# Performance work log

Hardware: AMD Instinct MI355X
Metric: run time of the kernel (lower is better)

The kernel has to match this reference:

```python
import jax, jax.numpy as jnp
import numpy as np

SIZE = 640
FPN_STRIDES = (8, 16, 32, 64, 128)
REG_MAX = 16
NUM_CLASSES = 80
TOPK = 45


def _build_anchors():
    pts, boxes, strides = [], [], []
    for s in FPN_STRIDES:
        h, w = SIZE // s, SIZE // s
        y, x = np.meshgrid(np.arange(h), np.arange(w), indexing='ij')
        yf = y.ravel().astype(np.float32)
        xf = x.ravel().astype(np.float32)
        pts.append(np.stack([(yf + 0.5) * s, (xf + 0.5) * s], -1))
        boxes.append(np.stack([yf * s, xf * s, (yf + 1) * s, (xf + 1) * s], -1))
        strides.append(np.full(h * w, s, np.float32))
    return (jnp.asarray(np.concatenate(pts), jnp.float32),
            jnp.asarray(np.concatenate(boxes), jnp.float32),
            jnp.asarray(np.concatenate(strides), jnp.float32))


ANCHOR_PTS, ANCHOR_BOXES, STRIDES = _build_anchors()
NUM_ANCHORS = ANCHOR_PTS.shape[0]  # 8525


def _iou(b1, b2):
    # elementwise IoU over trailing dim 4 in (y1, x1, y2, x2); axes are symmetric
    ty = jnp.maximum(b1[..., 0], b2[..., 0])
    tx = jnp.maximum(b1[..., 1], b2[..., 1])
    by = jnp.minimum(b1[..., 2], b2[..., 2])
    bx = jnp.minimum(b1[..., 3], b2[..., 3])
    inter = jnp.clip(by - ty, 0.0) * jnp.clip(bx - tx, 0.0)
    a1 = (b1[..., 2] - b1[..., 0]) * (b1[..., 3] - b1[..., 1])
    a2 = (b2[..., 2] - b2[..., 0]) * (b2[..., 3] - b2[..., 1])
    return inter / (a1 + a2 - inter)


def _assign_single(gt_cls, gt_bbox, pred_d):
    # gt_cls: (N,), gt_bbox: (N,4), pred_d: (4,A)
    A, N, C = NUM_ANCHORS, gt_bbox.shape[0], NUM_CLASSES
    pts, boxes, strides = ANCHOR_PTS, ANCHOR_BOXES, STRIDES
    centers = (gt_bbox[:, :2] + gt_bbox[:, 2:]) / 2
    dist = jnp.linalg.norm(centers[:, None, :] - pts[None, :, :], axis=-1)  # (N,A)
    _, k_ind = jax.lax.top_k(-dist, TOPK)  # (N,K) nearest anchors
    kb = boxes[k_ind]  # (N,K,4)
    Dg = _iou(gt_bbox[:, None, :], kb)  # (N,K)
    tg = Dg.mean(1) + Dg.std(1, ddof=1)  # torch .std() is unbiased
    ap = pts[k_ind]  # (N,K,2)
    inside = ((gt_bbox[:, None, 0] <= ap[..., 0]) & (ap[..., 0] <= gt_bbox[:, None, 2]) &
              (gt_bbox[:, None, 1] <= ap[..., 1]) & (ap[..., 1] <= gt_bbox[:, None, 3]))
    valid = (Dg >= tg[:, None]) & inside  # (N,K)
    n_idx = jnp.broadcast_to(jnp.arange(N, dtype=jnp.int32)[:, None], (N, TOPK))
    pri = jnp.where(valid, n_idx, -1).ravel()
    a_flat = k_ind.ravel()
    win_d = jnp.full((A,), -1, jnp.int32).at[a_flat].max(pri)
    wb = gt_bbox[jnp.clip(win_d, 0)]  # (A,4)
    gt_d = jnp.stack([(pts[:, 0] - wb[:, 0]) / strides,
                      (pts[:, 1] - wb[:, 1]) / strides,
                      (wb[:, 2] - pts[:, 0]) / strides,
                      (wb[:, 3] - pts[:, 1]) / strides], 0)  # (4,A) = [dtop,dleft,dbottom,dright]
    gt_dfl = jnp.where(win_d[None, :] >= 0, gt_d, jnp.inf)
    cls_pair = gt_cls.astype(jnp.int32)[n_idx]  # (N,K)
    ca = (cls_pair * A + k_ind).ravel()
    win_q = jnp.full((C * A,), -1, jnp.int32).at[ca].max(pri).reshape(C, A)
    gbq = gt_bbox[jnp.clip(win_q, 0)]  # (C,A,4)
    # _overlap_tlbr: decode(gt_d)*stride around anchor point, clamped -> clipped gt box
    box1 = jnp.clip(gbq, 0.0, float(SIZE))  # (C,A,4)
    rd = pred_d * strides[None, :]  # (4,A) raw offsets
    box2 = jnp.stack([jnp.clip(pts[:, 0] - rd[0], 0.0, float(SIZE)),
                      jnp.clip(pts[:, 1] - rd[1], 0.0, float(SIZE)),
                      jnp.clip(pts[:, 0] + rd[2], 0.0, float(SIZE)),
                      jnp.clip(pts[:, 1] + rd[3], 0.0, float(SIZE))], -1)  # (A,4)
    q = _iou(box1, box2[None, :, :])  # (C,A)
    gt_qfl = jnp.where(win_q >= 0, q, 0.0)
    return gt_qfl, gt_dfl


def setup_inputs() -> dict:
    key = jax.random.key(0)
    k1, k2, k3, k4 = jax.random.split(key, 4)
    B, N = 16, 64
    tl = jax.random.uniform(k1, (B, N, 2), jnp.float32, 0.0, SIZE - 64.0)
    wh = jax.random.uniform(k2, (B, N, 2), jnp.float32, 16.0, 256.0)
    br = jnp.minimum(tl + wh, float(SIZE))
    gt_bboxes = jnp.concatenate([tl, br], -1)  # (y1,x1,y2,x2)
    gt_clses = jax.random.randint(k3, (B, N), 0, NUM_CLASSES)
    pred_reg = jax.random.normal(k4, (B, 4, REG_MAX + 1, NUM_ANCHORS), jnp.float32)
    return {"gt_clses_batch": gt_clses, "gt_bboxes_batch": gt_bboxes,
            "pred_reg_batch": pred_reg}


def reference(gt_clses_batch, gt_bboxes_batch, pred_reg_batch):
    p = jax.nn.softmax(pred_reg_batch, axis=2)
    rng = jnp.arange(REG_MAX + 1, dtype=p.dtype).reshape(1, 1, -1, 1)
    pred_d = (p * rng).sum(2)  # (B,4,A) integral distribution -> expected offsets
    qfl, dfl = jax.vmap(_assign_single)(gt_clses_batch, gt_bboxes_batch, pred_d)
    return qfl, dfl, ANCHOR_PTS, STRIDES
```

## Files before the change

kernel.cpp:

```cpp
#include <hip/hip_runtime.h>
#include <math.h>
#include <float.h>

#define A_TOTAL 8525
#define NUM_B   16
#define NUM_N   64
#define NUM_C   80
#define K_TOP   45
#define SIZE_F  640.0f

#define UNASSIGNED_SENTINEL 1.0e30f

#define CUTOFF_KEY 0x43000000u
#define NBINS_PAD  2304
#define CAND_MAX   768

#define QFL_FLOATS  ((size_t)NUM_B * NUM_C * A_TOTAL)
#define DFL_FLOATS  ((size_t)NUM_B * 4 * A_TOTAL)
#define MASK_WORDS  (NUM_B * A_TOTAL)
#define MASK_VEC4   ((MASK_WORDS * 2) / 4)
#define QFL_VEC4    (QFL_FLOATS / 4)
#define DFL_VEC4    (DFL_FLOATS / 4)

__device__ __forceinline__ void anchor_decode(int a, float& py, float& px, float& s,
                                              float& qy0, float& qx0, float& qy1, float& qx1) {
    int rel, w; float sf;
    if (a < 6400)      { rel = a;        w = 80; sf = 8.f;   }
    else if (a < 8000) { rel = a - 6400; w = 40; sf = 16.f;  }
    else if (a < 8400) { rel = a - 8000; w = 20; sf = 32.f;  }
    else if (a < 8500) { rel = a - 8400; w = 10; sf = 64.f;  }
    else               { rel = a - 8500; w = 5;  sf = 128.f; }
    int y = rel / w, x = rel - y * w;
    float yf = (float)y, xf = (float)x;
    py  = (yf + 0.5f) * sf;  px  = (xf + 0.5f) * sf;
    qy0 = yf * sf;           qx0 = xf * sf;
    qy1 = (yf + 1.f) * sf;   qx1 = (xf + 1.f) * sf;
    s = sf;
}

__device__ __forceinline__ unsigned int dist_key_yx(int yy, int xx, float s,
                                                    float cy, float cx) {
    float py = __fmul_rn(__fadd_rn((float)yy, 0.5f), s);
    float px = __fmul_rn(__fadd_rn((float)xx, 0.5f), s);
    float dy = __fadd_rn(cy, -py);
    float dx = __fadd_rn(cx, -px);
    float v = sqrtf(__fadd_rn(__fmul_rn(dy, dy), __fmul_rn(dx, dx)));
    return __float_as_uint(v);
}

__device__ __forceinline__ float iou_box(float ay0, float ax0, float ay1, float ax1,
                                         float by0, float bx0, float by1, float bx1) {
    float ty = fmaxf(ay0, by0), tx = fmaxf(ax0, bx0);
    float by = fminf(ay1, by1), bx = fminf(ax1, bx1);
    float ih = fmaxf(__fadd_rn(by, -ty), 0.f);
    float iw = fmaxf(__fadd_rn(bx, -tx), 0.f);
    float inter = __fmul_rn(ih, iw);
    float a1 = __fmul_rn(__fadd_rn(ay1, -ay0), __fadd_rn(ax1, -ax0));
    float a2 = __fmul_rn(__fadd_rn(by1, -by0), __fadd_rn(bx1, -bx0));
    return inter / __fadd_rn(__fadd_rn(a1, a2), -inter);
}

__global__ __launch_bounds__(256) void prep_kernel(unsigned long long* __restrict__ mask,
                                                   float* __restrict__ qfl,
                                                   float* __restrict__ dfl,
                                                   float* __restrict__ opts,
                                                   float* __restrict__ ostr) {
    size_t gid = (size_t)blockIdx.x * 256 + threadIdx.x;
    size_t nthreads = (size_t)gridDim.x * 256;

    const uint4 z4 = make_uint4(0u, 0u, 0u, 0u);
    uint4* q4 = (uint4*)qfl;
    for (size_t i = gid; i < QFL_VEC4; i += nthreads)
        q4[i] = z4;

    const unsigned int su = __float_as_uint(UNASSIGNED_SENTINEL);
    const uint4 s4 = make_uint4(su, su, su, su);
    uint4* d4 = (uint4*)dfl;
    for (size_t i = gid; i < DFL_VEC4; i += nthreads)
        d4[i] = s4;

    uint4* m4 = (uint4*)mask;
    for (size_t i = gid; i < MASK_VEC4; i += nthreads)
        m4[i] = z4;

    for (size_t a = gid; a < A_TOTAL; a += nthreads) {
        float py, px, s, q0, q1, q2, q3;
        anchor_decode((int)a, py, px, s, q0, q1, q2, q3);
        opts[2 * a]     = py;
        opts[2 * a + 1] = px;
        ostr[a]         = s;
    }
}

__global__ __launch_bounds__(256) void assign_kernel(const float* __restrict__ gt_bbox,
                                                     unsigned long long* __restrict__ mask) {
    __shared__ unsigned int hist[NBINS_PAD];
    __shared__ unsigned int wtot[4];
    __shared__ unsigned int cand_key[CAND_MAX];
    __shared__ int          cand_idx[CAND_MAX];
    __shared__ int          s_candn;
    __shared__ int          s_B;
    __shared__ int          sel[K_TOP];
    __shared__ float        dg[K_TOP];
    __shared__ float        s_tg;

    const int   LH[5] = {80, 40, 20, 10, 5};
    const int   LB[5] = {0, 6400, 8000, 8400, 8500};
    const float LS[5] = {8.f, 16.f, 32.f, 64.f, 128.f};

    int tid = threadIdx.x;
    int lane = tid & 63, wid = tid >> 6;
    int b = blockIdx.x >> 6;
    int n = blockIdx.x & 63;
    const float* gb = gt_bbox + (size_t)(b * NUM_N + n) * 4;
    float g0 = gb[0], g1 = gb[1], g2 = gb[2], g3 = gb[3];
    float cy = __fmul_rn(__fadd_rn(g0, g2), 0.5f);
    float cx = __fmul_rn(__fadd_rn(g1, g3), 0.5f);

    int wy0[5], wx0[5], wnc[5], wcl[5];
#pragma unroll
    for (int l = 0; l < 5; ++l) {
        float s = LS[l]; int H = LH[l];
        int y0 = (int)((cy - 68.f) / s) - 1; if (y0 < 0) y0 = 0;
        int y1 = (int)((cy + 68.f) / s) + 1; if (y1 > H - 1) y1 = H - 1;
        int x0 = (int)((cx - 68.f) / s) - 1; if (x0 < 0) x0 = 0;
        int x1 = (int)((cx + 68.f) / s) + 1; if (x1 > H - 1) x1 = H - 1;
        wy0[l] = y0; wx0[l] = x0;
        wnc[l] = x1 - x0 + 1;
        wcl[l] = (y1 - y0 + 1) * wnc[l];
    }

    for (int i = tid; i < NBINS_PAD; i += 256) hist[i] = 0u;
    if (tid == 0) s_candn = 0;
    __syncthreads();

#pragma unroll
    for (int l = 0; l < 5; ++l) {
        int nc = wnc[l], cells = wcl[l];
        for (int t = tid; t < cells; t += 256) {
            int r = t / nc, c = t - r * nc;
            unsigned int key = dist_key_yx(wy0[l] + r, wx0[l] + c, LS[l], cy, cx);
            if (key < CUTOFF_KEY) atomicAdd(&hist[key >> 19], 1u);
        }
    }
    __syncthreads();

    unsigned int psum = 0;
    int base = tid * 9;
#pragma unroll
    for (int k = 0; k < 9; ++k) psum += hist[base + k];
    unsigned int x = psum;
    for (int off = 1; off < 64; off <<= 1) {
        unsigned int y = __shfl_up(x, off, 64);
        if (lane >= off) x += y;
    }
    if (lane == 63) wtot[wid] = x;
    __syncthreads();
    unsigned int wbase = 0;
    for (int w = 0; w < 4; ++w) wbase += (w < wid) ? wtot[w] : 0u;
    unsigned int inc = wbase + x;
    unsigned int exc = inc - psum;
    if (exc < (unsigned)K_TOP && inc >= (unsigned)K_TOP) {
        unsigned int cum = exc;
        int bbin = base;
        while (cum + hist[bbin] < (unsigned)K_TOP) { cum += hist[bbin]; ++bbin; }
        s_B = bbin;
    }
    __syncthreads();

    int B = s_B;
#pragma unroll
    for (int l = 0; l < 5; ++l) {
        int nc = wnc[l], cells = wcl[l];
        for (int t = tid; t < cells; t += 256) {
            int r = t / nc, c = t - r * nc;
            int yy = wy0[l] + r, xx = wx0[l] + c;
            unsigned int key = dist_key_yx(yy, xx, LS[l], cy, cx);
            if (key < CUTOFF_KEY && (int)(key >> 19) <= B) {
                int pos = atomicAdd(&s_candn, 1);
                if (pos < CAND_MAX) {
                    cand_key[pos] = key;
                    cand_idx[pos] = LB[l] + yy * LH[l] + xx;
                }
            }
        }
    }
    __syncthreads();

    int M = s_candn < CAND_MAX ? s_candn : CAND_MAX;
    for (int i = tid; i < M; i += 256) {
        unsigned int ki = cand_key[i]; int ii = cand_idx[i];
        int rank = 0;
        for (int j = 0; j < M; ++j) {
            unsigned int kj = cand_key[j]; int ij = cand_idx[j];
            rank += (kj < ki || (kj == ki && ij < ii)) ? 1 : 0;
        }
        if (rank < K_TOP) sel[rank] = ii;
    }
    __syncthreads();

    if (tid < K_TOP) {
        int a = sel[tid];
        float py, px, s, q0, q1, q2, q3;
        anchor_decode(a, py, px, s, q0, q1, q2, q3);
        dg[tid] = iou_box(g0, g1, g2, g3, q0, q1, q2, q3);
    }
    __syncthreads();
    if (tid == 0) {
        float sum = 0.f;
        for (int k = 0; k < K_TOP; ++k) sum = __fadd_rn(sum, dg[k]);
        float mean = sum / (float)K_TOP;
        float ss = 0.f;
        for (int k = 0; k < K_TOP; ++k) {
            float d = __fadd_rn(dg[k], -mean);
            ss = __fadd_rn(ss, __fmul_rn(d, d));
        }
        s_tg = __fadd_rn(mean, sqrtf(ss / (float)(K_TOP - 1)));
    }
    __syncthreads();
    if (tid < K_TOP) {
        int a = sel[tid];
        float py, px, s, q0, q1, q2, q3;
        anchor_decode(a, py, px, s, q0, q1, q2, q3);
        bool inside = (g0 <= py) && (py <= g2) && (g1 <= px) && (px <= g3);
        if (inside && dg[tid] >= s_tg) {
            atomicOr(&mask[(size_t)b * A_TOTAL + a], 1ull << n);
        }
    }
}

__global__ __launch_bounds__(256) void output_kernel(const int* __restrict__ gt_cls,
                                                     const float* __restrict__ gt_bbox,
                                                     const float* __restrict__ pred_reg,
                                                     const unsigned long long* __restrict__ mask,
                                                     float* __restrict__ qfl,
                                                     float* __restrict__ dfl) {
    __shared__ float s_gb[NUM_N * 4];
    __shared__ float s_gc[NUM_N * 4];
    __shared__ int   s_cls[NUM_N];

    int tid = threadIdx.x;
    int b = blockIdx.y;
    if (tid < NUM_N * 4) {
        float v = gt_bbox[(size_t)b * NUM_N * 4 + tid];
        s_gb[tid] = v;
        s_gc[tid] = fminf(fmaxf(v, 0.f), SIZE_F);
    }
    if (tid < NUM_N) s_cls[tid] = gt_cls[b * NUM_N + tid];
    __syncthreads();

    int a = blockIdx.x * 256 + tid;
    if (a >= A_TOTAL) return;

    unsigned long long m64 = mask[(size_t)b * A_TOTAL + a];
    if (m64 == 0ull) return;

    float* dflp = dfl + (size_t)b * 4 * A_TOTAL + a;
    float* qflp = qfl + (size_t)b * NUM_C * A_TOTAL + a;

    float py, px, s, q0, q1, q2, q3;
    anchor_decode(a, py, px, s, q0, q1, q2, q3);

    float rd[4];
    const float* pr = pred_reg + (size_t)b * 4 * 17 * A_TOTAL + a;
#pragma unroll
    for (int d = 0; d < 4; ++d) {
        float xv[17];
#pragma unroll
        for (int j = 0; j < 17; ++j) xv[j] = pr[(size_t)(d * 17 + j) * A_TOTAL];
        float m = xv[0];
#pragma unroll
        for (int j = 1; j < 17; ++j) m = fmaxf(m, xv[j]);
        float S = 0.f, dot = 0.f;
#pragma unroll
        for (int j = 0; j < 17; ++j) {
            float t = __expf(xv[j] - m);
            S += t;
            dot += t * (float)j;
        }
        rd[d] = (dot / S) * s;
    }
    float b2y0 = fminf(fmaxf(py - rd[0], 0.f), SIZE_F);
    float b2x0 = fminf(fmaxf(px - rd[1], 0.f), SIZE_F);
    float b2y1 = fminf(fmaxf(py + rd[2], 0.f), SIZE_F);
    float b2x1 = fminf(fmaxf(px + rd[3], 0.f), SIZE_F);

    {
        int n = 63 - __clzll(m64);
        dflp[0]            = (py - s_gb[n * 4 + 0]) / s;
        dflp[A_TOTAL]      = (px - s_gb[n * 4 + 1]) / s;
        dflp[2 * A_TOTAL]  = (s_gb[n * 4 + 2] - py) / s;
        dflp[3 * A_TOTAL]  = (s_gb[n * 4 + 3] - px) / s;
    }

    unsigned long long seen0 = 0ull, seen1 = 0ull;
    unsigned long long mm = m64;
    while (mm) {
        int n = 63 - __clzll(mm);
        mm &= ~(1ull << n);
        int c = s_cls[n];
        bool done;
        if (c < 64) {
            unsigned long long bit = 1ull << c;
            done = (seen0 & bit) != 0ull; seen0 |= bit;
        } else {
            unsigned long long bit = 1ull << (c - 64);
            done = (seen1 & bit) != 0ull; seen1 |= bit;
        }
        if (!done) {
            qflp[(size_t)c * A_TOTAL] = iou_box(s_gc[n * 4 + 0], s_gc[n * 4 + 1],
                                                s_gc[n * 4 + 2], s_gc[n * 4 + 3],
                                                b2y0, b2x0, b2y1, b2x1);
        }
    }
}

extern "C" void kernel_launch(void* const* d_in, const int* in_sizes, int n_in,
                              void* d_out, int out_size, void* d_ws, size_t ws_size,
                              hipStream_t stream) {
    const int*   gt_cls   = (const int*)d_in[0];
    const float* gt_bbox  = (const float*)d_in[1];
    const float* pred_reg = (const float*)d_in[2];

    float* qfl  = (float*)d_out;
    float* dfl  = qfl + QFL_FLOATS;
    float* opts = dfl + DFL_FLOATS;
    float* ostr = opts + (size_t)A_TOTAL * 2;

    unsigned long long* mask = (unsigned long long*)d_ws;

    hipLaunchKernelGGL(prep_kernel, dim3(2048), dim3(256), 0, stream,
                       mask, qfl, dfl, opts, ostr);
    hipLaunchKernelGGL(assign_kernel, dim3(NUM_B * NUM_N), dim3(256), 0, stream, gt_bbox, mask);
    hipLaunchKernelGGL(output_kernel, dim3((A_TOTAL + 255) / 256, NUM_B), dim3(256), 0, stream,
                       gt_cls, gt_bbox, pred_reg, mask, qfl, dfl);
}
```

Baseline: 112.0 us.

## Fold output zero-fill into assign kernel and compact assigned anchors into worklist

The large qfl/dfl initialization and anchor-point writes move from the prep kernel into the assign kernel. There they overlap with the per-GT top-k selection instead of running as a separate bandwidth-bound pass, and prep now only clears the mask. The assign kernel also appends each newly assigned (batch, anchor) pair to a global worklist via atomicAdd, so the output kernel walks only assigned anchors with a grid-stride loop instead of scanning all of them. This adds an atomic counter and makes the output kernel stage all batches' GT data into shared memory per block.

```diff
diff --git a/kernel.cpp b/kernel.cpp
--- a/kernel.cpp
+++ b/kernel.cpp
@@ -18,9 +18,13 @@
 #define QFL_FLOATS  ((size_t)NUM_B * NUM_C * A_TOTAL)
 #define DFL_FLOATS  ((size_t)NUM_B * 4 * A_TOTAL)
 #define MASK_WORDS  (NUM_B * A_TOTAL)
+#define MASK_BYTES  ((size_t)MASK_WORDS * 8)
 #define MASK_VEC4   ((MASK_WORDS * 2) / 4)
 #define QFL_VEC4    (QFL_FLOATS / 4)
 #define DFL_VEC4    (DFL_FLOATS / 4)
+#define WL_CAP      (NUM_B * NUM_N * K_TOP)
+
+#define ASSIGN_BLOCKS (NUM_B * NUM_N)
 
 __device__ __forceinline__ void anchor_decode(int a, float& py, float& px, float& s,
                                               float& qy0, float& qx0, float& qy1, float& qx1) {
@@ -61,39 +65,24 @@
 }
 
 __global__ __launch_bounds__(256) void prep_kernel(unsigned long long* __restrict__ mask,
-                                                   float* __restrict__ qfl,
-                                                   float* __restrict__ dfl,
-                                                   float* __restrict__ opts,
-                                                   float* __restrict__ ostr) {
+                                                   int* __restrict__ wcount) {
     size_t gid = (size_t)blockIdx.x * 256 + threadIdx.x;
     size_t nthreads = (size_t)gridDim.x * 256;
-
+    if (gid == 0) *wcount = 0;
+    uint4* m4 = (uint4*)mask;
     const uint4 z4 = make_uint4(0u, 0u, 0u, 0u);
-    uint4* q4 = (uint4*)qfl;
-    for (size_t i = gid; i < QFL_VEC4; i += nthreads)
-        q4[i] = z4;
-
-    const unsigned int su = __float_as_uint(UNASSIGNED_SENTINEL);
-    const uint4 s4 = make_uint4(su, su, su, su);
-    uint4* d4 = (uint4*)dfl;
-    for (size_t i = gid; i < DFL_VEC4; i += nthreads)
-        d4[i] = s4;
-
-    uint4* m4 = (uint4*)mask;
     for (size_t i = gid; i < MASK_VEC4; i += nthreads)
         m4[i] = z4;
-
-    for (size_t a = gid; a < A_TOTAL; a += nthreads) {
-        float py, px, s, q0, q1, q2, q3;
-        anchor_decode((int)a, py, px, s, q0, q1, q2, q3);
-        opts[2 * a]     = py;
-        opts[2 * a + 1] = px;
-        ostr[a]         = s;
-    }
 }
 
 __global__ __launch_bounds__(256) void assign_kernel(const float* __restrict__ gt_bbox,
-                                                     unsigned long long* __restrict__ mask) {
+                                                     unsigned long long* __restrict__ mask,
+                                                     int* __restrict__ wcount,
+                                                     int* __restrict__ wlist,
+                                                     float* __restrict__ qfl,
+                                                     float* __restrict__ dfl,
+                                                     float* __restrict__ opts,
+                                                     float* __restrict__ ostr) {
     __shared__ unsigned int hist[NBINS_PAD];
     __shared__ unsigned int wtot[4];
     __shared__ unsigned int cand_key[CAND_MAX];
@@ -109,6 +98,31 @@
     const float LS[5] = {8.f, 16.f, 32.f, 64.f, 128.f};
 
     int tid = threadIdx.x;
+
+    {
+        size_t gid = (size_t)blockIdx.x * 256 + tid;
+        const size_t nthreads = (size_t)ASSIGN_BLOCKS * 256;
+
+        const uint4 z4 = make_uint4(0u, 0u, 0u, 0u);
+        uint4* q4 = (uint4*)qfl;
+        for (size_t i = gid; i < QFL_VEC4; i += nthreads)
+            q4[i] = z4;
+
+        const unsigned int su = __float_as_uint(UNASSIGNED_SENTINEL);
+        const uint4 s4 = make_uint4(su, su, su, su);
+        uint4* d4 = (uint4*)dfl;
+        for (size_t i = gid; i < DFL_VEC4; i += nthreads)
+            d4[i] = s4;
+
+        for (size_t a = gid; a < A_TOTAL; a += nthreads) {
+            float py, px, s, q0, q1, q2, q3;
+            anchor_decode((int)a, py, px, s, q0, q1, q2, q3);
+            opts[2 * a]     = py;
+            opts[2 * a + 1] = px;
+            ostr[a]         = s;
+        }
+    }
+
     int lane = tid & 63, wid = tid >> 6;
     int b = blockIdx.x >> 6;
     int n = blockIdx.x & 63;
@@ -224,7 +238,12 @@
         anchor_decode(a, py, px, s, q0, q1, q2, q3);
         bool inside = (g0 <= py) && (py <= g2) && (g1 <= px) && (px <= g3);
         if (inside && dg[tid] >= s_tg) {
-            atomicOr(&mask[(size_t)b * A_TOTAL + a], 1ull << n);
+            unsigned long long old =
+                atomicOr(&mask[(size_t)b * A_TOTAL + a], 1ull << n);
+            if (old == 0ull) {
+                int p = atomicAdd(wcount, 1);
+                wlist[p] = b * A_TOTAL + a;
+            }
         }
     }
 }
@@ -233,84 +252,88 @@
                                                      const float* __restrict__ gt_bbox,
                                                      const float* __restrict__ pred_reg,
                                                      const unsigned long long* __restrict__ mask,
+                                                     const int* __restrict__ wcount,
+                                                     const int* __restrict__ wlist,
                                                      float* __restrict__ qfl,
                                                      float* __restrict__ dfl) {
-    __shared__ float s_gb[NUM_N * 4];
-    __shared__ float s_gc[NUM_N * 4];
-    __shared__ int   s_cls[NUM_N];
+    __shared__ float s_gb[NUM_B * NUM_N * 4];
+    __shared__ float s_gc[NUM_B * NUM_N * 4];
+    __shared__ int   s_cls[NUM_B * NUM_N];
 
     int tid = threadIdx.x;
-    int b = blockIdx.y;
-    if (tid < NUM_N * 4) {
-        float v = gt_bbox[(size_t)b * NUM_N * 4 + tid];
-        s_gb[tid] = v;
-        s_gc[tid] = fminf(fmaxf(v, 0.f), SIZE_F);
-    }
-    if (tid < NUM_N) s_cls[tid] = gt_cls[b * NUM_N + tid];
-    __syncthreads();
-
-    int a = blockIdx.x * 256 + tid;
-    if (a >= A_TOTAL) return;
-
-    unsigned long long m64 = mask[(size_t)b * A_TOTAL + a];
-    if (m64 == 0ull) return;
-
-    float* dflp = dfl + (size_t)b * 4 * A_TOTAL + a;
-    float* qflp = qfl + (size_t)b * NUM_C * A_TOTAL + a;
-
-    float py, px, s, q0, q1, q2, q3;
-    anchor_decode(a, py, px, s, q0, q1, q2, q3);
-
-    float rd[4];
-    const float* pr = pred_reg + (size_t)b * 4 * 17 * A_TOTAL + a;
-#pragma unroll
-    for (int d = 0; d < 4; ++d) {
-        float xv[17];
-#pragma unroll
-        for (int j = 0; j < 17; ++j) xv[j] = pr[(size_t)(d * 17 + j) * A_TOTAL];
-        float m = xv[0];
-#pragma unroll
-        for (int j = 1; j < 17; ++j) m = fmaxf(m, xv[j]);
-        float S = 0.f, dot = 0.f;
-#pragma unroll
-        for (int j = 0; j < 17; ++j) {
-            float t = __expf(xv[j] - m);
-            S += t;
-            dot += t * (float)j;
-        }
-        rd[d] = (dot / S) * s;
-    }
-    float b2y0 = fminf(fmaxf(py - rd[0], 0.f), SIZE_F);
-    float b2x0 = fminf(fmaxf(px - rd[1], 0.f), SIZE_F);
-    float b2y1 = fminf(fmaxf(py + rd[2], 0.f), SIZE_F);
-    float b2x1 = fminf(fmaxf(px + rd[3], 0.f), SIZE_F);
-
-    {
-        int n = 63 - __clzll(m64);
-        dflp[0]            = (py - s_gb[n * 4 + 0]) / s;
-        dflp[A_TOTAL]      = (px - s_gb[n * 4 + 1]) / s;
-        dflp[2 * A_TOTAL]  = (s_gb[n * 4 + 2] - py) / s;
-        dflp[3 * A_TOTAL]  = (s_gb[n * 4 + 3] - px) / s;
-    }
-
-    unsigned long long seen0 = 0ull, seen1 = 0ull;
-    unsigned long long mm = m64;
-    while (mm) {
-        int n = 63 - __clzll(mm);
-        mm &= ~(1ull << n);
-        int c = s_cls[n];
-        bool done;
-        if (c < 64) {
-            unsigned long long bit = 1ull << c;
-            done = (seen0 & bit) != 0ull; seen0 |= bit;
-        } else {
-            unsigned long long bit = 1ull << (c - 64);
-            done = (seen1 & bit) != 0ull; seen1 |= bit;
-        }
-        if (!done) {
-            qflp[(size_t)c * A_TOTAL] = iou_box(s_gc[n * 4 + 0], s_gc[n * 4 + 1],
-                                                s_gc[n * 4 + 2], s_gc[n * 4 + 3],
-                                                b2y0, b2x0, b2y1, b2x1);
+    for (int i = tid; i < NUM_B * NUM_N * 4; i += 256) {
+        float v = gt_bbox[i];
+        s_gb[i] = v;
+        s_gc[i] = fminf(fmaxf(v, 0.f), SIZE_F);
+    }
+    for (int i = tid; i < NUM_B * NUM_N; i += 256) s_cls[i] = gt_cls[i];
+    __syncthreads();
+
+    int total = *wcount;
+    for (int i = blockIdx.x * 256 + tid; i < total; i += gridDim.x * 256) {
+        int e = wlist[i];
+        int b = e / A_TOTAL;
+        int a = e - b * A_TOTAL;
+        unsigned long long m64 = mask[e];
+
+        float py, px, s, q0, q1, q2, q3;
+        anchor_decode(a, py, px, s, q0, q1, q2, q3);
+
+        float* dflp = dfl + (size_t)b * 4 * A_TOTAL + a;
+        float* qflp = qfl + (size_t)b * NUM_C * A_TOTAL + a;
+
+        float rd[4];
+        const float* pr = pred_reg + (size_t)b * 4 * 17 * A_TOTAL + a;
+#pragma unroll
+        for (int d = 0; d < 4; ++d) {
+            float xv[17];
+#pragma unroll
+            for (int j = 0; j < 17; ++j) xv[j] = pr[(size_t)(d * 17 + j) * A_TOTAL];
+            float m = xv[0];
+#pragma unroll
+            for (int j = 1; j < 17; ++j) m = fmaxf(m, xv[j]);
+            float S = 0.f, dot = 0.f;
+#pragma unroll
+            for (int j = 0; j < 17; ++j) {
+                float t = __expf(xv[j] - m);
+                S += t;
+                dot += t * (float)j;
+            }
+            rd[d] = (dot / S) * s;
+        }
+        float b2y0 = fminf(fmaxf(py - rd[0], 0.f), SIZE_F);
+        float b2x0 = fminf(fmaxf(px - rd[1], 0.f), SIZE_F);
+        float b2y1 = fminf(fmaxf(py + rd[2], 0.f), SIZE_F);
+        float b2x1 = fminf(fmaxf(px + rd[3], 0.f), SIZE_F);
+
+        {
+            int n = 63 - __clzll(m64);
+            const float* g = s_gb + (size_t)(b * NUM_N + n) * 4;
+            dflp[0]            = (py - g[0]) / s;
+            dflp[A_TOTAL]      = (px - g[1]) / s;
+            dflp[2 * A_TOTAL]  = (g[2] - py) / s;
+            dflp[3 * A_TOTAL]  = (g[3] - px) / s;
+        }
+
+        unsigned long long seen0 = 0ull, seen1 = 0ull;
+        unsigned long long mm = m64;
+        while (mm) {
+            int n = 63 - __clzll(mm);
+            mm &= ~(1ull << n);
+            int c = s_cls[b * NUM_N + n];
+            bool done;
+            if (c < 64) {
+                unsigned long long bit = 1ull << c;
+                done = (seen0 & bit) != 0ull; seen0 |= bit;
+            } else {
+                unsigned long long bit = 1ull << (c - 64);
+                done = (seen1 & bit) != 0ull; seen1 |= bit;
+            }
+            if (!done) {
+                const float* g = s_gc + (size_t)(b * NUM_N + n) * 4;
+                qflp[(size_t)c * A_TOTAL] = iou_box(g[0], g[1], g[2], g[3],
+                                                    b2y0, b2x0, b2y1, b2x1);
+            }
         }
     }
 }
@@ -328,10 +351,12 @@
     float* ostr = opts + (size_t)A_TOTAL * 2;
 
     unsigned long long* mask = (unsigned long long*)d_ws;
-
-    hipLaunchKernelGGL(prep_kernel, dim3(2048), dim3(256), 0, stream,
-                       mask, qfl, dfl, opts, ostr);
-    hipLaunchKernelGGL(assign_kernel, dim3(NUM_B * NUM_N), dim3(256), 0, stream, gt_bbox, mask);
-    hipLaunchKernelGGL(output_kernel, dim3((A_TOTAL + 255) / 256, NUM_B), dim3(256), 0, stream,
-                       gt_cls, gt_bbox, pred_reg, mask, qfl, dfl);
-}
+    int* wcount = (int*)((char*)d_ws + MASK_BYTES);
+    int* wlist  = wcount + 1;
+
+    hipLaunchKernelGGL(prep_kernel, dim3(64), dim3(256), 0, stream, mask, wcount);
+    hipLaunchKernelGGL(assign_kernel, dim3(ASSIGN_BLOCKS), dim3(256), 0, stream,
+                       gt_bbox, mask, wcount, wlist, qfl, dfl, opts, ostr);
+    hipLaunchKernelGGL(output_kernel, dim3(256), dim3(256), 0, stream,
+                       gt_cls, gt_bbox, pred_reg, mask, wcount, wlist, qfl, dfl);
+}
```

Result: slower. 137.4 us (+22.7%).

## Fuse output zero-fill into assign kernel and split softmax per direction

Applied to the files above, without the earlier changes.

Moves the large qfl zeroing, dfl sentinel fill and anchor output writes from the prep kernel into the assign kernel, so this bulk store traffic overlaps with the assign kernel's histogram/top-k work. The prep kernel now only clears the mask. The output kernel is remapped so each of the four wavefronts computes the 17-bin softmax for one regression direction over 64 anchors. Results go through shared memory, and wavefront 0 then writes the IoU scores. This gives four times more threads for the softmax loads, at the cost of an extra barrier and idle wavefronts during the qfl scatter.

```diff
diff --git a/kernel.cpp b/kernel.cpp
--- a/kernel.cpp
+++ b/kernel.cpp
@@ -21,6 +21,8 @@
 #define MASK_VEC4   ((MASK_WORDS * 2) / 4)
 #define QFL_VEC4    (QFL_FLOATS / 4)
 #define DFL_VEC4    (DFL_FLOATS / 4)
+
+#define ASSIGN_BLOCKS (NUM_B * NUM_N)
 
 __device__ __forceinline__ void anchor_decode(int a, float& py, float& px, float& s,
                                               float& qy0, float& qx0, float& qy1, float& qx1) {
@@ -60,40 +62,21 @@
     return inter / __fadd_rn(__fadd_rn(a1, a2), -inter);
 }
 
-__global__ __launch_bounds__(256) void prep_kernel(unsigned long long* __restrict__ mask,
-                                                   float* __restrict__ qfl,
-                                                   float* __restrict__ dfl,
-                                                   float* __restrict__ opts,
-                                                   float* __restrict__ ostr) {
+__global__ __launch_bounds__(256) void prep_kernel(unsigned long long* __restrict__ mask) {
     size_t gid = (size_t)blockIdx.x * 256 + threadIdx.x;
     size_t nthreads = (size_t)gridDim.x * 256;
-
+    uint4* m4 = (uint4*)mask;
     const uint4 z4 = make_uint4(0u, 0u, 0u, 0u);
-    uint4* q4 = (uint4*)qfl;
-    for (size_t i = gid; i < QFL_VEC4; i += nthreads)
-        q4[i] = z4;
-
-    const unsigned int su = __float_as_uint(UNASSIGNED_SENTINEL);
-    const uint4 s4 = make_uint4(su, su, su, su);
-    uint4* d4 = (uint4*)dfl;
-    for (size_t i = gid; i < DFL_VEC4; i += nthreads)
-        d4[i] = s4;
-
-    uint4* m4 = (uint4*)mask;
     for (size_t i = gid; i < MASK_VEC4; i += nthreads)
         m4[i] = z4;
-
-    for (size_t a = gid; a < A_TOTAL; a += nthreads) {
-        float py, px, s, q0, q1, q2, q3;
-        anchor_decode((int)a, py, px, s, q0, q1, q2, q3);
-        opts[2 * a]     = py;
-        opts[2 * a + 1] = px;
-        ostr[a]         = s;
-    }
 }
 
 __global__ __launch_bounds__(256) void assign_kernel(const float* __restrict__ gt_bbox,
-                                                     unsigned long long* __restrict__ mask) {
+                                                     unsigned long long* __restrict__ mask,
+                                                     float* __restrict__ qfl,
+                                                     float* __restrict__ dfl,
+                                                     float* __restrict__ opts,
+                                                     float* __restrict__ ostr) {
     __shared__ unsigned int hist[NBINS_PAD];
     __shared__ unsigned int wtot[4];
     __shared__ unsigned int cand_key[CAND_MAX];
@@ -109,6 +92,31 @@
     const float LS[5] = {8.f, 16.f, 32.f, 64.f, 128.f};
 
     int tid = threadIdx.x;
+
+    {
+        size_t gid = (size_t)blockIdx.x * 256 + tid;
+        const size_t nthreads = (size_t)ASSIGN_BLOCKS * 256;
+
+        const uint4 z4 = make_uint4(0u, 0u, 0u, 0u);
+        uint4* q4 = (uint4*)qfl;
+        for (size_t i = gid; i < QFL_VEC4; i += nthreads)
+            q4[i] = z4;
+
+        const unsigned int su = __float_as_uint(UNASSIGNED_SENTINEL);
+        const uint4 s4 = make_uint4(su, su, su, su);
+        uint4* d4 = (uint4*)dfl;
+        for (size_t i = gid; i < DFL_VEC4; i += nthreads)
+            d4[i] = s4;
+
+        for (size_t a = gid; a < A_TOTAL; a += nthreads) {
+            float py, px, s, q0, q1, q2, q3;
+            anchor_decode((int)a, py, px, s, q0, q1, q2, q3);
+            opts[2 * a]     = py;
+            opts[2 * a + 1] = px;
+            ostr[a]         = s;
+        }
+    }
+
     int lane = tid & 63, wid = tid >> 6;
     int b = blockIdx.x >> 6;
     int n = blockIdx.x & 63;
@@ -238,9 +246,14 @@
     __shared__ float s_gb[NUM_N * 4];
     __shared__ float s_gc[NUM_N * 4];
     __shared__ int   s_cls[NUM_N];
-
-    int tid = threadIdx.x;
-    int b = blockIdx.y;
+    __shared__ float s_rd[4][64];
+
+    int tid  = threadIdx.x;
+    int lane = tid & 63;
+    int d    = tid >> 6;
+    int b    = blockIdx.y;
+    int a    = blockIdx.x * 64 + lane;
+
     if (tid < NUM_N * 4) {
         float v = gt_bbox[(size_t)b * NUM_N * 4 + tid];
         s_gb[tid] = v;
@@ -249,25 +262,18 @@
     if (tid < NUM_N) s_cls[tid] = gt_cls[b * NUM_N + tid];
     __syncthreads();
 
-    int a = blockIdx.x * 256 + tid;
-    if (a >= A_TOTAL) return;
-
-    unsigned long long m64 = mask[(size_t)b * A_TOTAL + a];
-    if (m64 == 0ull) return;
-
-    float* dflp = dfl + (size_t)b * 4 * A_TOTAL + a;
-    float* qflp = qfl + (size_t)b * NUM_C * A_TOTAL + a;
+    unsigned long long m64 = 0ull;
+    if (a < A_TOTAL) m64 = mask[(size_t)b * A_TOTAL + a];
+    bool active = (m64 != 0ull);
 
     float py, px, s, q0, q1, q2, q3;
-    anchor_decode(a, py, px, s, q0, q1, q2, q3);
-
-    float rd[4];
-    const float* pr = pred_reg + (size_t)b * 4 * 17 * A_TOTAL + a;
-#pragma unroll
-    for (int d = 0; d < 4; ++d) {
+    anchor_decode(a < A_TOTAL ? a : 0, py, px, s, q0, q1, q2, q3);
+
+    if (active) {
+        const float* pr = pred_reg + ((size_t)b * 4 + d) * 17 * A_TOTAL + a;
         float xv[17];
 #pragma unroll
-        for (int j = 0; j < 17; ++j) xv[j] = pr[(size_t)(d * 17 + j) * A_TOTAL];
+        for (int j = 0; j < 17; ++j) xv[j] = pr[(size_t)j * A_TOTAL];
         float m = xv[0];
 #pragma unroll
         for (int j = 1; j < 17; ++j) m = fmaxf(m, xv[j]);
@@ -278,39 +284,48 @@
             S += t;
             dot += t * (float)j;
         }
-        rd[d] = (dot / S) * s;
-    }
-    float b2y0 = fminf(fmaxf(py - rd[0], 0.f), SIZE_F);
-    float b2x0 = fminf(fmaxf(px - rd[1], 0.f), SIZE_F);
-    float b2y1 = fminf(fmaxf(py + rd[2], 0.f), SIZE_F);
-    float b2x1 = fminf(fmaxf(px + rd[3], 0.f), SIZE_F);
-
-    {
+        s_rd[d][lane] = (dot / S) * s;
+
         int n = 63 - __clzll(m64);
-        dflp[0]            = (py - s_gb[n * 4 + 0]) / s;
-        dflp[A_TOTAL]      = (px - s_gb[n * 4 + 1]) / s;
-        dflp[2 * A_TOTAL]  = (s_gb[n * 4 + 2] - py) / s;
-        dflp[3 * A_TOTAL]  = (s_gb[n * 4 + 3] - px) / s;
-    }
-
-    unsigned long long seen0 = 0ull, seen1 = 0ull;
-    unsigned long long mm = m64;
-    while (mm) {
-        int n = 63 - __clzll(mm);
-        mm &= ~(1ull << n);
-        int c = s_cls[n];
-        bool done;
-        if (c < 64) {
-            unsigned long long bit = 1ull << c;
-            done = (seen0 & bit) != 0ull; seen0 |= bit;
-        } else {
-            unsigned long long bit = 1ull << (c - 64);
-            done = (seen1 & bit) != 0ull; seen1 |= bit;
-        }
-        if (!done) {
-            qflp[(size_t)c * A_TOTAL] = iou_box(s_gc[n * 4 + 0], s_gc[n * 4 + 1],
-                                                s_gc[n * 4 + 2], s_gc[n * 4 + 3],
-                                                b2y0, b2x0, b2y1, b2x1);
+        const float* g = s_gb + n * 4;
+        float v;
+        if      (d == 0) v = (py - g[0]) / s;
+        else if (d == 1) v = (px - g[1]) / s;
+        else if (d == 2) v = (g[2] - py) / s;
+        else             v = (g[3] - px) / s;
+        dfl[((size_t)b * 4 + d) * A_TOTAL + a] = v;
+    }
+    __syncthreads();
+
+    if (active && d == 0) {
+        float r0 = s_rd[0][lane], r1 = s_rd[1][lane];
+        float r2 = s_rd[2][lane], r3 = s_rd[3][lane];
+        float b2y0 = fminf(fmaxf(py - r0, 0.f), SIZE_F);
+        float b2x0 = fminf(fmaxf(px - r1, 0.f), SIZE_F);
+        float b2y1 = fminf(fmaxf(py + r2, 0.f), SIZE_F);
+        float b2x1 = fminf(fmaxf(px + r3, 0.f), SIZE_F);
+
+        float* qflp = qfl + (size_t)b * NUM_C * A_TOTAL + a;
+
+        unsigned long long seen0 = 0ull, seen1 = 0ull;
+        unsigned long long mm = m64;
+        while (mm) {
+            int n = 63 - __clzll(mm);
+            mm &= ~(1ull << n);
+            int c = s_cls[n];
+            bool done;
+            if (c < 64) {
+                unsigned long long bit = 1ull << c;
+                done = (seen0 & bit) != 0ull; seen0 |= bit;
+            } else {
+                unsigned long long bit = 1ull << (c - 64);
+                done = (seen1 & bit) != 0ull; seen1 |= bit;
+            }
+            if (!done) {
+                const float* g = s_gc + n * 4;
+                qflp[(size_t)c * A_TOTAL] = iou_box(g[0], g[1], g[2], g[3],
+                                                    b2y0, b2x0, b2y1, b2x1);
+            }
         }
     }
 }
@@ -329,9 +344,9 @@
 
     unsigned long long* mask = (unsigned long long*)d_ws;
 
-    hipLaunchKernelGGL(prep_kernel, dim3(2048), dim3(256), 0, stream,
-                       mask, qfl, dfl, opts, ostr);
-    hipLaunchKernelGGL(assign_kernel, dim3(NUM_B * NUM_N), dim3(256), 0, stream, gt_bbox, mask);
-    hipLaunchKernelGGL(output_kernel, dim3((A_TOTAL + 255) / 256, NUM_B), dim3(256), 0, stream,
+    hipLaunchKernelGGL(prep_kernel, dim3(64), dim3(256), 0, stream, mask);
+    hipLaunchKernelGGL(assign_kernel, dim3(ASSIGN_BLOCKS), dim3(256), 0, stream,
+                       gt_bbox, mask, qfl, dfl, opts, ostr);
+    hipLaunchKernelGGL(output_kernel, dim3((A_TOTAL + 63) / 64, NUM_B), dim3(256), 0, stream,
                        gt_cls, gt_bbox, pred_reg, mask, qfl, dfl);
 }
```

Result: faster. 109.7 us, median of 2 (-2.1%).
